# Performance work log

Measured on AMD Instinct MI355X. Metric: run time of the kernel, lower is better.

The kernel has to match this reference:

```python
import jax, jax.numpy as jnp
import numpy as np
from jax import lax

EPS = 1e-5

def binarize_ste(x):
    # sign binarization to {-1,+1} (0 -> +1) with straight-through gradient
    s = jnp.where(x >= 0, 1.0, -1.0).astype(x.dtype)
    return x + lax.stop_gradient(s - x)

def bn(x, gamma, beta, mean, var):
    # inference-mode batchnorm; broadcast over channel axis 1 for 4D, axis 1 for 2D
    if x.ndim == 4:
        shape = (1, -1, 1, 1)
    else:
        shape = (1, -1)
    inv = gamma.reshape(shape) / jnp.sqrt(var.reshape(shape) + EPS)
    return (x - mean.reshape(shape)) * inv + beta.reshape(shape)

def conv_rep(x, w):
    # replicate (edge) padding of 1, then valid 3x3 conv, NCHW/OIHW
    xp = jnp.pad(x, ((0, 0), (0, 0), (1, 1), (1, 1)), mode='edge')
    return lax.conv_general_dilated(xp, binarize_ste(w), (1, 1), 'VALID',
                                    dimension_numbers=('NCHW', 'OIHW', 'NCHW'))

def maxpool2(x):
    return lax.reduce_window(x, -jnp.inf, lax.max, (1, 1, 2, 2), (1, 1, 2, 2), 'VALID')

def hardtanh(x):
    return jnp.clip(x, -1.0, 1.0)

def setup_inputs() -> dict:
    key = jax.random.key(0)
    ks = jax.random.split(key, 16)
    B = 2048
    inp = {
        'x': jax.random.normal(ks[0], (B, 1, 28, 28), jnp.float32),
        'conv1_w': jax.random.normal(ks[1], (64, 1, 3, 3), jnp.float32),
        'bn1_gamma': jax.random.uniform(ks[2], (64,), jnp.float32),
        'bn1_beta': jax.random.normal(ks[3], (64,), jnp.float32),
        'bn1_mean': jax.random.normal(ks[4], (64,), jnp.float32),
        'bn1_var': jax.random.uniform(ks[5], (64,), jnp.float32),
        'conv2_w': jax.random.normal(ks[6], (64, 64, 3, 3), jnp.float32),
        'bn2_gamma': jax.random.uniform(ks[7], (64,), jnp.float32),
        'bn2_beta': jax.random.normal(ks[8], (64,), jnp.float32),
        'bn2_mean': jax.random.normal(ks[9], (64,), jnp.float32),
        'bn2_var': jax.random.uniform(ks[10], (64,), jnp.float32),
        'fc1_w': jax.random.normal(ks[11], (2048, 3136), jnp.float32),
        'bn3_gamma': jax.random.uniform(ks[12], (2048,), jnp.float32),
        'bn3_beta': jax.random.normal(ks[13], (2048,), jnp.float32),
        'bn3_mean': jax.random.normal(ks[14], (2048,), jnp.float32),
        'bn3_var': jax.random.uniform(ks[15], (2048,), jnp.float32),
        'fc2_w': jax.random.normal(jax.random.fold_in(key, 99), (10, 2048), jnp.float32),
        'scale': jnp.array([0.001], jnp.float32),
    }
    return inp

def reference(x, conv1_w, bn1_gamma, bn1_beta, bn1_mean, bn1_var,
              conv2_w, bn2_gamma, bn2_beta, bn2_mean, bn2_var,
              fc1_w, bn3_gamma, bn3_beta, bn3_mean, bn3_var,
              fc2_w, scale):
    # block 1: binarized conv -> BN -> hardtanh -> binarize -> maxpool
    h = conv_rep(x, conv1_w)                          # [B,64,28,28]
    h = binarize_ste(hardtanh(bn(h, bn1_gamma, bn1_beta, bn1_mean, bn1_var)))
    h = maxpool2(h)                                   # [B,64,14,14]
    # block 2
    h = conv_rep(h, conv2_w)                          # [B,64,14,14]
    h = binarize_ste(hardtanh(bn(h, bn2_gamma, bn2_beta, bn2_mean, bn2_var)))
    h = maxpool2(h)                                   # [B,64,7,7]
    h = h.reshape(h.shape[0], -1)                     # [B,3136] (C*H*W order)
    # fc block
    h = h @ binarize_ste(fc1_w).T                     # [B,2048]
    h = binarize_ste(hardtanh(bn(h, bn3_gamma, bn3_beta, bn3_mean, bn3_var)))
    h = h @ binarize_ste(fc2_w).T                     # [B,10]
    return h * scale
```

## Files before the change

kernel.cpp:

```cpp
#include <hip/hip_runtime.h>
#include <cstdint>

#define EPS 1e-5f

typedef unsigned long long u64;
typedef unsigned int u32;
typedef unsigned short u16;
typedef unsigned char u8;

__device__ __forceinline__ int clampi(int v, int lo, int hi) {
    return v < lo ? lo : (v > hi ? hi : v);
}


__global__ __launch_bounds__(256) void prep_all(
    const float* __restrict__ fc1_w,
    const float* __restrict__ conv1_w, const float* __restrict__ conv2_w,
    const float* __restrict__ fc2_w,
    const float* __restrict__ g1, const float* __restrict__ b1,
    const float* __restrict__ m1, const float* __restrict__ v1,
    const float* __restrict__ g2, const float* __restrict__ b2,
    const float* __restrict__ m2, const float* __restrict__ v2,
    u64* __restrict__ wp,
    float* __restrict__ s1, u64* __restrict__ w2p, u64* __restrict__ w2pk,
    float4* __restrict__ bnc1, float4* __restrict__ bnc2)
{
    __shared__ float ls[3136];
    int blk = blockIdx.x;
    int tid = threadIdx.x;

    if (blk < 2048) {
        int o = blk;
        const float4* row4 = (const float4*)(fc1_w + o * 3136);
        for (int i = tid; i < 784; i += 256)
            ((float4*)ls)[i] = row4[i];
        __syncthreads();
        int wave = tid >> 6, lane = tid & 63;
        for (int p = wave; p < 49; p += 4) {
            u64 ball = __ballot(ls[lane * 49 + p] >= 0.f);
            if (lane == 0) wp[p * 2048 + o] = ball;
        }
        return;
    }

    int t = (blk - 2048) * 256 + tid;
    if (t < 576) {
        s1[t] = (conv1_w[t] >= 0.f) ? 1.f : -1.f;
    } else if (t < 1152) {
        int u = t - 576;
        int co = u / 9, tap = u % 9;
        u64 word = 0;
        for (int ci = 0; ci < 64; ci++)
            word |= (u64)(conv2_w[(co * 64 + ci) * 9 + tap] >= 0.f) << ci;
        w2p[u] = word;
    } else if (t < 1472) {
        int u = t - 1152;
        int o = u / 32, k = u % 32;
        u64 word = 0;
        for (int j = 0; j < 64; j++)
            word |= (u64)(fc2_w[o * 2048 + k * 64 + j] >= 0.f) << j;
        w2pk[u] = word;
    } else if (t < 1536) {
        int ch = t - 1472;
        bnc1[ch] = make_float4(m1[ch], g1[ch] / sqrtf(v1[ch] + EPS), b1[ch], 0.f);
    } else if (t < 1600) {
        int ch = t - 1536;
        bnc2[ch] = make_float4(m2[ch], g2[ch] / sqrtf(v2[ch] + EPS), b2[ch], 0.f);
    }
}


__global__ __launch_bounds__(256) void k_conv1(
    const float* __restrict__ x, const float* __restrict__ s1,
    const float4* __restrict__ bnc1, u64* __restrict__ out1)
{
    int tid = threadIdx.x;
    int g = blockIdx.y;
    int base = g * 16;

    int idx = blockIdx.x * 256 + tid;
    int b = idx / 196, p = idx % 196;
    int pi = p / 14, pj = p % 14;

    const float* xb = x + b * 784;
    int rr[4], cc[4];
    #pragma unroll
    for (int r = 0; r < 4; r++) rr[r] = clampi(2 * pi - 1 + r, 0, 27) * 28;
    #pragma unroll
    for (int c = 0; c < 4; c++) cc[c] = clampi(2 * pj - 1 + c, 0, 27);
    float patch[4][4];
    #pragma unroll
    for (int r = 0; r < 4; r++)
        #pragma unroll
        for (int c = 0; c < 4; c++)
            patch[r][c] = xb[rr[r] + cc[c]];

    u32 word = 0;
    #pragma unroll 4
    for (int ch = 0; ch < 16; ch++) {
        const float* w = s1 + (base + ch) * 9;
        float v00 = 0.f, v01 = 0.f, v10 = 0.f, v11 = 0.f;
        #pragma unroll
        for (int ki = 0; ki < 3; ki++)
            #pragma unroll
            for (int kj = 0; kj < 3; kj++) {
                float ww = w[ki * 3 + kj];
                v00 += patch[ki][kj] * ww;
                v01 += patch[ki][kj + 1] * ww;
                v10 += patch[ki + 1][kj] * ww;
                v11 += patch[ki + 1][kj + 1] * ww;
            }
        float vmin = fminf(fminf(v00, v01), fminf(v10, v11));
        float vmax = fmaxf(fmaxf(v00, v01), fmaxf(v10, v11));
        float4 c4 = bnc1[base + ch];
        float vsel = (c4.y >= 0.f) ? vmax : vmin;
        int bit = ((vsel - c4.x) * c4.y + c4.z) >= 0.f;
        word |= (u32)bit << ch;
    }
    ((u16*)out1)[idx * 4 + g] = (u16)word;
}


__global__ __launch_bounds__(256) void k_conv2(
    const u64* __restrict__ in, const u64* __restrict__ w2p,
    const float4* __restrict__ bnc2, u64* __restrict__ out2)
{
    int tid = threadIdx.x;
    int g = blockIdx.y;
    int base = g * 8;

    int idx = blockIdx.x * 256 + tid;
    int b = idx / 49, p = idx % 49;
    int pi = p / 7, pj = p % 7;

    const u64* ib = in + b * 196;
    int rr[4], cc[4];
    #pragma unroll
    for (int r = 0; r < 4; r++) rr[r] = clampi(2 * pi - 1 + r, 0, 13) * 14;
    #pragma unroll
    for (int c = 0; c < 4; c++) cc[c] = clampi(2 * pj - 1 + c, 0, 13);
    u64 a[4][4];
    #pragma unroll
    for (int r = 0; r < 4; r++)
        #pragma unroll
        for (int c = 0; c < 4; c++)
            a[r][c] = ib[rr[r] + cc[c]];

    u32 word = 0;
    #pragma unroll
    for (int co = 0; co < 8; co++) {
        const u64* w = w2p + (base + co) * 9;
        int s00 = 0, s01 = 0, s10 = 0, s11 = 0;
        #pragma unroll
        for (int ki = 0; ki < 3; ki++)
            #pragma unroll
            for (int kj = 0; kj < 3; kj++) {
                u64 ww = w[ki * 3 + kj];
                s00 += __popcll(a[ki][kj] ^ ww);
                s01 += __popcll(a[ki][kj + 1] ^ ww);
                s10 += __popcll(a[ki + 1][kj] ^ ww);
                s11 += __popcll(a[ki + 1][kj + 1] ^ ww);
            }
        int smin = min(min(s00, s01), min(s10, s11));
        int smax = max(max(s00, s01), max(s10, s11));
        float4 c4 = bnc2[base + co];
        int ssel = (c4.y >= 0.f) ? smin : smax;
        int bit = (((float)(576 - 2 * ssel) - c4.x) * c4.y + c4.z) >= 0.f;
        word |= (u32)bit << co;
    }
    ((u8*)out2)[idx * 8 + g] = (u8)word;
}


#define NB 8

__global__ __launch_bounds__(256) void k_fc1(
    const u64* __restrict__ act, const u64* __restrict__ wp,
    const float* __restrict__ g, const float* __restrict__ bt,
    const float* __restrict__ mn, const float* __restrict__ vr,
    u64* __restrict__ out3)
{
    int tid = threadIdx.x;
    int btile = blockIdx.x >> 3;
    int otile = blockIdx.x & 7;
    int b0 = btile * NB;
    int o = otile * 256 + tid;
    const u64* ab = act + b0 * 49;

    int sums[NB];
    #pragma unroll
    for (int i = 0; i < NB; i++) sums[i] = 0;

    for (int p = 0; p < 49; p++) {
        u64 w = wp[p * 2048 + o];
        #pragma unroll
        for (int bb = 0; bb < NB; bb++)
            sums[bb] += __popcll(ab[bb * 49 + p] ^ w);
    }

    float iv = g[o] / sqrtf(vr[o] + EPS);
    float m = mn[o], be = bt[o];
    #pragma unroll
    for (int bb = 0; bb < NB; bb++) {
        float y = ((float)(3136 - 2 * sums[bb]) - m) * iv + be;
        u64 ball = __ballot(y >= 0.f);
        if ((tid & 63) == 0) out3[(b0 + bb) * 32 + (o >> 6)] = ball;
    }
}


__global__ void k_fc2(const u64* __restrict__ act, const u64* __restrict__ w2,
                      const float* __restrict__ scale, float* __restrict__ out)
{
    int idx = blockIdx.x * 256 + threadIdx.x;
    if (idx >= 2048 * 16) return;
    int b = idx >> 4, o = idx & 15;
    if (o >= 10) return;
    int s = 0;
    #pragma unroll
    for (int k = 0; k < 32; k++)
        s += __popcll(act[b * 32 + k] ^ w2[o * 32 + k]);
    out[b * 10 + o] = scale[0] * (float)(2048 - 2 * s);
}


extern "C" void kernel_launch(void* const* d_in, const int* in_sizes, int n_in,
                              void* d_out, int out_size, void* d_ws, size_t ws_size,
                              hipStream_t stream) {
    const float* x        = (const float*)d_in[0];
    const float* conv1_w  = (const float*)d_in[1];
    const float* bn1_g    = (const float*)d_in[2];
    const float* bn1_b    = (const float*)d_in[3];
    const float* bn1_m    = (const float*)d_in[4];
    const float* bn1_v    = (const float*)d_in[5];
    const float* conv2_w  = (const float*)d_in[6];
    const float* bn2_g    = (const float*)d_in[7];
    const float* bn2_b    = (const float*)d_in[8];
    const float* bn2_m    = (const float*)d_in[9];
    const float* bn2_v    = (const float*)d_in[10];
    const float* fc1_w    = (const float*)d_in[11];
    const float* bn3_g    = (const float*)d_in[12];
    const float* bn3_b    = (const float*)d_in[13];
    const float* bn3_m    = (const float*)d_in[14];
    const float* bn3_v    = (const float*)d_in[15];
    const float* fc2_w    = (const float*)d_in[16];
    const float* scale    = (const float*)d_in[17];
    float* out = (float*)d_out;

    char* ws = (char*)d_ws;
    float*  s1   = (float*) (ws + 0);
    u64*    w2p  = (u64*)   (ws + 2560);
    float4* bnc1 = (float4*)(ws + 7168);
    u64*    wp   = (u64*)   (ws + 8192);
    u64*    w2pk = (u64*)   (ws + 811008);
    float4* bnc2 = (float4*)(ws + 813568);
    u64*    out1 = (u64*)   (ws + 819200);
    u64*    out2 = (u64*)   (ws + 4030464);
    u64*    out3 = (u64*)   (ws + 4833280);

    hipLaunchKernelGGL(prep_all, dim3(2055), dim3(256), 0, stream,
                       fc1_w, conv1_w, conv2_w, fc2_w,
                       bn1_g, bn1_b, bn1_m, bn1_v,
                       bn2_g, bn2_b, bn2_m, bn2_v,
                       wp, s1, w2p, w2pk, bnc1, bnc2);

    hipLaunchKernelGGL(k_conv1, dim3(1568, 4), dim3(256), 0, stream,
                       x, s1, bnc1, out1);
    hipLaunchKernelGGL(k_conv2, dim3(392, 8), dim3(256), 0, stream,
                       out1, w2p, bnc2, out2);
    hipLaunchKernelGGL(k_fc1, dim3(2048), dim3(256), 0, stream,
                       out2, wp, bn3_g, bn3_b, bn3_m, bn3_v, out3);
    hipLaunchKernelGGL(k_fc2, dim3(128), dim3(256), 0, stream,
                       out3, w2pk, scale, out);
}
```

Measured before the change: 210.0 us.

## Fuse fc1 and fc2 into one kernel with shared-memory bit handoff

Merges the binarized fc1 and fc2 kernels into a single kernel. Each 1024-thread block covers 8 batch rows and all 2048 outputs, with each thread computing two outputs. The fc1 sign bits are staged in shared memory and fc2 is computed in the same block, removing one launch and the global round trip of the intermediate activations. The grid shrinks from 2048 blocks to 256 large blocks, which lowers parallelism and could hurt latency hiding. The final fc2 stage runs on only 80 threads per block.

```diff
diff --git a/kernel.cpp b/kernel.cpp
--- a/kernel.cpp
+++ b/kernel.cpp
@@ -172,55 +172,58 @@
 }
 
 
-#define NB 8
-
-__global__ __launch_bounds__(256) void k_fc1(
+__global__ __launch_bounds__(1024) void k_fc12(
     const u64* __restrict__ act, const u64* __restrict__ wp,
     const float* __restrict__ g, const float* __restrict__ bt,
     const float* __restrict__ mn, const float* __restrict__ vr,
-    u64* __restrict__ out3)
-{
-    int tid = threadIdx.x;
-    int btile = blockIdx.x >> 3;
-    int otile = blockIdx.x & 7;
-    int b0 = btile * NB;
-    int o = otile * 256 + tid;
+    const u64* __restrict__ w2pk, const float* __restrict__ scale,
+    float* __restrict__ out)
+{
+    __shared__ u64 bits[8][32];
+    int tid = threadIdx.x;
+    int b0 = blockIdx.x * 8;
+    int oA = tid, oB = tid + 1024;
     const u64* ab = act + b0 * 49;
 
-    int sums[NB];
-    #pragma unroll
-    for (int i = 0; i < NB; i++) sums[i] = 0;
+    int sumsA[8], sumsB[8];
+    #pragma unroll
+    for (int i = 0; i < 8; i++) { sumsA[i] = 0; sumsB[i] = 0; }
 
     for (int p = 0; p < 49; p++) {
-        u64 w = wp[p * 2048 + o];
-        #pragma unroll
-        for (int bb = 0; bb < NB; bb++)
-            sums[bb] += __popcll(ab[bb * 49 + p] ^ w);
-    }
-
-    float iv = g[o] / sqrtf(vr[o] + EPS);
-    float m = mn[o], be = bt[o];
-    #pragma unroll
-    for (int bb = 0; bb < NB; bb++) {
-        float y = ((float)(3136 - 2 * sums[bb]) - m) * iv + be;
-        u64 ball = __ballot(y >= 0.f);
-        if ((tid & 63) == 0) out3[(b0 + bb) * 32 + (o >> 6)] = ball;
-    }
-}
-
-
-__global__ void k_fc2(const u64* __restrict__ act, const u64* __restrict__ w2,
-                      const float* __restrict__ scale, float* __restrict__ out)
-{
-    int idx = blockIdx.x * 256 + threadIdx.x;
-    if (idx >= 2048 * 16) return;
-    int b = idx >> 4, o = idx & 15;
-    if (o >= 10) return;
-    int s = 0;
-    #pragma unroll
-    for (int k = 0; k < 32; k++)
-        s += __popcll(act[b * 32 + k] ^ w2[o * 32 + k]);
-    out[b * 10 + o] = scale[0] * (float)(2048 - 2 * s);
+        u64 wA = wp[p * 2048 + oA];
+        u64 wB = wp[p * 2048 + oB];
+        #pragma unroll
+        for (int bb = 0; bb < 8; bb++) {
+            u64 aw = ab[bb * 49 + p];
+            sumsA[bb] += __popcll(aw ^ wA);
+            sumsB[bb] += __popcll(aw ^ wB);
+        }
+    }
+
+    float ivA = g[oA] / sqrtf(vr[oA] + EPS), mA = mn[oA], beA = bt[oA];
+    float ivB = g[oB] / sqrtf(vr[oB] + EPS), mB = mn[oB], beB = bt[oB];
+    int w = tid >> 6;
+    #pragma unroll
+    for (int bb = 0; bb < 8; bb++) {
+        float yA = ((float)(3136 - 2 * sumsA[bb]) - mA) * ivA + beA;
+        float yB = ((float)(3136 - 2 * sumsB[bb]) - mB) * ivB + beB;
+        u64 ballA = __ballot(yA >= 0.f);
+        u64 ballB = __ballot(yB >= 0.f);
+        if ((tid & 63) == 0) {
+            bits[bb][w] = ballA;
+            bits[bb][16 + w] = ballB;
+        }
+    }
+    __syncthreads();
+
+    if (tid < 80) {
+        int b = tid / 10, o = tid % 10;
+        int s = 0;
+        #pragma unroll
+        for (int k = 0; k < 32; k++)
+            s += __popcll(bits[b][k] ^ w2pk[o * 32 + k]);
+        out[(b0 + b) * 10 + o] = scale[0] * (float)(2048 - 2 * s);
+    }
 }
 
 
@@ -256,7 +259,6 @@
     float4* bnc2 = (float4*)(ws + 813568);
     u64*    out1 = (u64*)   (ws + 819200);
     u64*    out2 = (u64*)   (ws + 4030464);
-    u64*    out3 = (u64*)   (ws + 4833280);
 
     hipLaunchKernelGGL(prep_all, dim3(2055), dim3(256), 0, stream,
                        fc1_w, conv1_w, conv2_w, fc2_w,
@@ -268,8 +270,6 @@
                        x, s1, bnc1, out1);
     hipLaunchKernelGGL(k_conv2, dim3(392, 8), dim3(256), 0, stream,
                        out1, w2p, bnc2, out2);
-    hipLaunchKernelGGL(k_fc1, dim3(2048), dim3(256), 0, stream,
-                       out2, wp, bn3_g, bn3_b, bn3_m, bn3_v, out3);
-    hipLaunchKernelGGL(k_fc2, dim3(128), dim3(256), 0, stream,
-                       out3, w2pk, scale, out);
-}
+    hipLaunchKernelGGL(k_fc12, dim3(256), dim3(1024), 0, stream,
+                       out2, wp, bn3_g, bn3_b, bn3_m, bn3_v, w2pk, scale, out);
+}
```

New measurement: 210.1 us. No clear change (+0.0%).
